# Kernel optimization log

Measured on AMD Instinct MI355X. Metric: run time of the kernel, lower is better.

Reference implementation:

```python
import jax, jax.numpy as jnp
import numpy as np

N = 100000          # nodes
E = 1600000         # edges
D_IN = 128
HID = 256
N_CLASSES = 10
N_GRAPHS = 64


def gcn_conv(x, src, dst, W, b, n_nodes):
    """PyG GCNConv: add self-loops, symmetric deg^{-1/2} normalization, x@W, scatter-add."""
    h = x @ W  # [N, out]
    loop = jnp.arange(n_nodes, dtype=src.dtype)
    src2 = jnp.concatenate([src, loop])
    dst2 = jnp.concatenate([dst, loop])
    deg = jax.ops.segment_sum(jnp.ones(src2.shape[0], x.dtype), dst2, num_segments=n_nodes)
    dinv = jax.lax.rsqrt(deg)  # deg >= 1 thanks to self-loops
    norm = dinv[src2] * dinv[dst2]  # [E+N]
    msg = norm[:, None] * h[src2]   # [E+N, out]
    return jax.ops.segment_sum(msg, dst2, num_segments=n_nodes) + b


def setup_inputs() -> dict:
    key = jax.random.key(0)
    ks = jax.random.split(key, 12)
    x = jax.random.normal(ks[0], (N, D_IN), dtype=jnp.float32)
    edge_index = jax.random.randint(ks[1], (2, E), 0, N, dtype=jnp.int64)
    batch = jnp.sort(jax.random.randint(ks[2], (N,), 0, N_GRAPHS, dtype=jnp.int64))
    def glorot(k, shape):
        lim = float(np.sqrt(6.0 / (shape[0] + shape[1])))
        return jax.random.uniform(k, shape, jnp.float32, -lim, lim)
    W1 = glorot(ks[3], (D_IN, HID));  b1 = jnp.zeros((HID,), jnp.float32)
    W2 = glorot(ks[4], (HID, HID));   b2 = jnp.zeros((HID,), jnp.float32)
    Wf1 = glorot(ks[5], (HID, HID));  bf1 = jnp.zeros((HID,), jnp.float32)
    Wf2 = glorot(ks[6], (HID, N_CLASSES)); bf2 = jnp.zeros((N_CLASSES,), jnp.float32)
    return {"x": x, "edge_index": edge_index, "batch": batch,
            "W1": W1, "b1": b1, "W2": W2, "b2": b2,
            "Wf1": Wf1, "bf1": bf1, "Wf2": Wf2, "bf2": bf2}


def reference(x, edge_index, batch, W1, b1, W2, b2, Wf1, bf1, Wf2, bf2):
    src, dst = edge_index[0], edge_index[1]
    h = jax.nn.relu(gcn_conv(x, src, dst, W1, b1, N))
    h = jax.nn.relu(gcn_conv(h, src, dst, W2, b2, N))
    # global mean pool over graph ids
    summed = jax.ops.segment_sum(h, batch, num_segments=N_GRAPHS)  # [G, HID]
    counts = jax.ops.segment_sum(jnp.ones((N,), h.dtype), batch, num_segments=N_GRAPHS)
    pooled = summed / jnp.maximum(counts, 1.0)[:, None]
    z = jax.nn.relu(pooled @ Wf1 + bf1)
    alpha = jax.nn.softplus(z @ Wf2 + bf2) + 0.001
    return alpha
```

## Files before the change

### kernel.cpp

```cpp
#include <hip/hip_runtime.h>
#include <math.h>

#define NN   100000
#define NE   1600000
#define DIN  128
#define HID  256
#define NG   64
#define NCLS 10

#define NBLK 128
#define EPB  (NE / NBLK)
#define NBUK 512
#define NPB  196

using bf16x8 = __attribute__((ext_vector_type(8))) short;
using f32x4  = __attribute__((ext_vector_type(4))) float;
using f32x2  = __attribute__((ext_vector_type(2))) float;
using u32x2  = __attribute__((ext_vector_type(2))) unsigned int;

static __device__ __forceinline__ unsigned short f2bf(float f) {
    unsigned u = __float_as_uint(f);
    u += 0x7fff + ((u >> 16) & 1);
    return (unsigned short)(u >> 16);
}
static __device__ __forceinline__ float bf2f(unsigned short h) {
    return __uint_as_float(((unsigned)h) << 16);
}

static __device__ __forceinline__ unsigned char f32_to_fp8(float f) {
    float a = fminf(fabsf(f), 448.f);
    unsigned bits = __float_as_uint(a * 0x1p-120f);
    bits += 0x7ffff + ((bits >> 20) & 1);
    unsigned e4 = (bits >> 20) & 0x7f;
    return (unsigned char)(e4 | (f < 0.f ? 0x80u : 0u));
}
#if __has_builtin(__builtin_amdgcn_cvt_pk_f32_fp8)
#define HAVE_CVT_FP8 1
#endif
static __device__ __forceinline__ void fp8x4_to_f32(unsigned u, float* f) {
#ifdef HAVE_CVT_FP8
    f32x2 lo = __builtin_amdgcn_cvt_pk_f32_fp8((int)u, false);
    f32x2 hi = __builtin_amdgcn_cvt_pk_f32_fp8((int)u, true);
    f[0] = lo[0]; f[1] = lo[1]; f[2] = hi[0]; f[3] = hi[1];
#else
#pragma unroll
    for (int k = 0; k < 4; ++k) {
        unsigned b = (u >> (8 * k)) & 0xffu;
        unsigned bits = ((b & 0x80u) << 24) | ((b & 0x7fu) << 20);
        f[k] = __uint_as_float(bits) * 0x1p+120f;
    }
#endif
}


__global__ __launch_bounds__(256) void k_hist(const int* __restrict__ dst,
                                              int* __restrict__ histg) {
    __shared__ int h[NBUK];
    const int t = threadIdx.x;
    for (int i = t; i < NBUK; i += 256) h[i] = 0;
    __syncthreads();
    const int e0 = blockIdx.x * EPB, e1 = e0 + EPB;
    for (int e = e0 + t; e < e1; e += 256)
        atomicAdd(&h[(unsigned)__builtin_nontemporal_load(&dst[e]) / NPB], 1);
    __syncthreads();
    for (int i = t; i < NBUK; i += 256)
        histg[i * NBLK + blockIdx.x] = h[i];
}

__global__ __launch_bounds__(1024) void k_scan64k(int* __restrict__ d) {
    __shared__ int ts[1024];
    const int t = threadIdx.x;
    const int base = t * 64;
    int s = 0;
    for (int i = 0; i < 64; ++i) s += d[base + i];
    ts[t] = s;
    __syncthreads();
    for (int off = 1; off < 1024; off <<= 1) {
        int u = (t >= off) ? ts[t - off] : 0;
        __syncthreads();
        ts[t] += u;
        __syncthreads();
    }
    int run = ts[t] - s;
    for (int i = 0; i < 64; ++i) {
        int v = d[base + i];
        d[base + i] = run;
        run += v;
    }
}

__global__ __launch_bounds__(256) void k_scatter(const int* __restrict__ src,
                                                 const int* __restrict__ dst,
                                                 const int* __restrict__ offg,
                                                 int2* __restrict__ pairs) {
    __shared__ int cur[NBUK];
    const int t = threadIdx.x;
    for (int i = t; i < NBUK; i += 256) cur[i] = offg[i * NBLK + blockIdx.x];
    __syncthreads();
    const int e0 = blockIdx.x * EPB, e1 = e0 + EPB;
    for (int e = e0 + t; e < e1; e += 256) {
        int d = __builtin_nontemporal_load(&dst[e]);
        int sv = __builtin_nontemporal_load(&src[e]);
        int b = (unsigned)d / NPB;
        int p = atomicAdd(&cur[b], 1);
        u32x2 pv; pv.x = (unsigned)sv; pv.y = (unsigned)d;
        __builtin_nontemporal_store(pv, (u32x2*)&pairs[p]);
    }
}

__global__ __launch_bounds__(256) void k_csr(const int2* __restrict__ pairs,
                                             const int* __restrict__ offg,
                                             int* __restrict__ csr,
                                             int* __restrict__ deg,
                                             float* __restrict__ dinv,
                                             int* __restrict__ offs) {
    __shared__ int cnt[NPB];
    __shared__ int loff[256];
    __shared__ int cur[NPB];
    const int b = blockIdx.x, t = threadIdx.x;
    const int s     = offg[b * NBLK];
    const int e_end = (b == NBUK - 1) ? NE : offg[(b + 1) * NBLK];
    const int nb0   = b * NPB;
    const int nnod  = min(NPB, NN - nb0);
    if (t < NPB) cnt[t] = 0;
    __syncthreads();
    for (int e = s + t; e < e_end; e += 256)
        atomicAdd(&cnt[pairs[e].y - nb0], 1);
    __syncthreads();
    int v = (t < NPB) ? cnt[t] : 0;
    loff[t] = v;
    __syncthreads();
    for (int off = 1; off < 256; off <<= 1) {
        int u = (t >= off) ? loff[t - off] : 0;
        __syncthreads();
        loff[t] += u;
        __syncthreads();
    }
    int myoff = loff[t] - v;
    __syncthreads();
    loff[t] = myoff;
    if (t < NPB) cur[t] = 0;
    __syncthreads();
    if (t < nnod) {
        int node = nb0 + t;
        int dg = cnt[t];
        deg[node]  = dg;
        dinv[node] = rsqrtf((float)(dg + 1));
        offs[node] = s + myoff;
    }
    for (int e = s + t; e < e_end; e += 256) {
        int2 pr = pairs[e];
        int li = pr.y - nb0;
        int p = atomicAdd(&cur[li], 1);
        csr[s + loff[li] + p] = pr.x;
    }
}

__global__ void k_counts(const int* __restrict__ batch, float* __restrict__ countsf) {
    int g = threadIdx.x;
    if (g >= NG) return;
    int lo = 0, hi = NN;
    while (lo < hi) { int mid = (lo + hi) >> 1; if (batch[mid] < g) lo = mid + 1; else hi = mid; }
    int lb = lo;
    lo = 0; hi = NN;
    while (lo < hi) { int mid = (lo + hi) >> 1; if (batch[mid] <= g) lo = mid + 1; else hi = mid; }
    countsf[g] = (float)(lo - lb);
}


__global__ void k_cast_x8(const float* __restrict__ x, const float* __restrict__ dinv,
                          unsigned char* __restrict__ xs8, int nq) {
    int i = blockIdx.x * blockDim.x + threadIdx.x;
    if (i >= nq) return;
    int nd = i >> 5;
    int q  = i & 31;
    float dv = dinv[nd];
    const float4 v = *(const float4*)&x[(size_t)nd * DIN + q * 4];
    uchar4 o;
    o.x = f32_to_fp8(v.x * dv); o.y = f32_to_fp8(v.y * dv);
    o.z = f32_to_fp8(v.z * dv); o.w = f32_to_fp8(v.w * dv);
    *(uchar4*)&xs8[(size_t)nd * DIN + q * 4] = o;
}

__global__ void k_cast_wt2(const float* __restrict__ W1, unsigned short* __restrict__ Wt1,
                           const float* __restrict__ W2, unsigned short* __restrict__ Wt2) {
    int i = blockIdx.x * blockDim.x + threadIdx.x;
    if (i < DIN * HID) {
        int k = i >> 8, nc = i & 255;
        Wt1[nc * DIN + k] = f2bf(W1[i]);
    } else if (i < (DIN + HID) * HID) {
        int j = i - DIN * HID;
        int k = j >> 8, nc = j & 255;
        Wt2[nc * HID + k] = f2bf(W2[j]);
    }
}


template <int MODE>
__global__ __launch_bounds__(256) void k_gemm_mfma(const unsigned short* __restrict__ A,
                                                   const unsigned short* __restrict__ Wt,
                                                   const float* __restrict__ dinv,
                                                   const float* __restrict__ bias,
                                                   void* __restrict__ outp,
                                                   const int* __restrict__ batch,
                                                   float* __restrict__ pooled,
                                                   int M, int K) {
    __shared__ unsigned short As[128 * 40];
    __shared__ unsigned short Bs[128 * 40];
    __shared__ float psum[4][128];
    __shared__ int gloc[128];
    const int t = threadIdx.x;
    const int lane = t & 63;
    const int wid = t >> 6;
    const int wr = wid >> 1, wc = wid & 1;
    const int bm = blockIdx.x * 128, bn = blockIdx.y * 128;
    const int lr = lane & 15;
    const int ko = (lane >> 4) << 3;

    f32x4 acc[4][4] = {};

    const int r = t >> 2;
    const int kq = (t & 3) << 3;

    int g0 = 0;
    if (MODE == 2) {
        g0 = batch[bm];
        for (int i = t; i < 4 * 128; i += 256) ((float*)psum)[i] = 0.f;
        if (t < 128) gloc[t] = (bm + t < M) ? (batch[bm + t] - g0) : 0;
    }

    for (int kk = 0; kk < K; kk += 32) {
#pragma unroll
        for (int h = 0; h < 128; h += 64) {
            int row = bm + r + h;
            int4 v = make_int4(0, 0, 0, 0);
            if (row < M) v = *(const int4*)&A[(size_t)row * K + kk + kq];
            *(int4*)&As[(r + h) * 40 + kq] = v;
        }
#pragma unroll
        for (int h = 0; h < 128; h += 64) {
            int nrow = bn + r + h;
            int4 v = *(const int4*)&Wt[(size_t)nrow * K + kk + kq];
            *(int4*)&Bs[(r + h) * 40 + kq] = v;
        }
        __syncthreads();
        bf16x8 af[4], bfr[4];
#pragma unroll
        for (int mf = 0; mf < 4; ++mf)
            af[mf] = *(const bf16x8*)&As[(wr * 64 + mf * 16 + lr) * 40 + ko];
#pragma unroll
        for (int nf = 0; nf < 4; ++nf)
            bfr[nf] = *(const bf16x8*)&Bs[(wc * 64 + nf * 16 + lr) * 40 + ko];
#pragma unroll
        for (int mf = 0; mf < 4; ++mf)
#pragma unroll
            for (int nf = 0; nf < 4; ++nf)
                acc[mf][nf] = __builtin_amdgcn_mfma_f32_16x16x32_bf16(af[mf], bfr[nf], acc[mf][nf], 0, 0, 0);
        __syncthreads();
    }

    if (MODE == 1) {
        unsigned char* out8 = (unsigned char*)outp;
#pragma unroll
        for (int mf = 0; mf < 4; ++mf) {
#pragma unroll
            for (int b = 0; b < 4; ++b) {
                int row = bm + wr * 64 + mf * 16 + (lane >> 4) * 4 + b;
                if (row >= M) continue;
                float dv = dinv[row];
#pragma unroll
                for (int nf = 0; nf < 4; ++nf) {
                    int col = bn + wc * 64 + nf * 16 + lr;
                    float v = fmaxf(acc[mf][nf][b] + bias[col], 0.f);
                    out8[(size_t)row * HID + col] = f32_to_fp8(dv * v);
                }
            }
        }
    } else {
        const int q4 = (lane >> 4) << 2;
#pragma unroll
        for (int nf = 0; nf < 4; ++nf) {
            const int lcol = wc * 64 + nf * 16 + lr;
            const float bb = bias[bn + lcol];
            float run = 0.f; int gcur = 0;
#pragma unroll
            for (int mf = 0; mf < 4; ++mf) {
#pragma unroll
                for (int b = 0; b < 4; ++b) {
                    int lrow = wr * 64 + mf * 16 + q4 + b;
                    if (bm + lrow < M) {
                        int gl = gloc[lrow];
                        float v = fmaxf(acc[mf][nf][b] + bb, 0.f);
                        if (gl != gcur) {
                            if (run != 0.f) {
                                if (gcur < 4) atomicAdd(&psum[gcur][lcol], run);
                                else atomicAdd(&pooled[(size_t)(g0 + gcur) * HID + bn + lcol], run);
                            }
                            run = 0.f; gcur = gl;
                        }
                        run += v;
                    }
                }
            }
            if (run != 0.f) {
                if (gcur < 4) atomicAdd(&psum[gcur][lcol], run);
                else atomicAdd(&pooled[(size_t)(g0 + gcur) * HID + bn + lcol], run);
            }
        }
        __syncthreads();
        for (int i = t; i < 4 * 128; i += 256) {
            int gl = i >> 7, lcol = i & 127;
            int g = g0 + gl;
            float v = psum[gl][lcol];
            if (g < NG && v != 0.f)
                atomicAdd(&pooled[(size_t)g * HID + bn + lcol], v);
        }
    }
}


__global__ __launch_bounds__(256) void k_agg256(const unsigned char* __restrict__ hs,
                                                const int* __restrict__ csr,
                                                const int* __restrict__ offs,
                                                const int* __restrict__ deg,
                                                const float* __restrict__ dinv,
                                                unsigned short* __restrict__ out, int n) {
    int wid = threadIdx.x >> 6, lane = threadIdx.x & 63;
    int node = blockIdx.x * 4 + wid;
    if (node >= n) return;
    int c = lane << 2;
    float a0, a1, a2, a3;
    {
        unsigned u = *(const unsigned*)&hs[(size_t)node * HID + c];
        float f[4]; fp8x4_to_f32(u, f);
        a0 = f[0]; a1 = f[1]; a2 = f[2]; a3 = f[3];
    }
    int s0 = offs[node], cnt = deg[node];
    for (int base = 0; base < cnt; base += 64) {
        int nb = min(64, cnt - base);
        int idx = (lane < nb) ? __builtin_nontemporal_load(&csr[s0 + base + lane]) : 0;
        int i = 0;
        for (; i + 8 <= nb; i += 8) {
            unsigned v[8];
#pragma unroll
            for (int k = 0; k < 8; ++k) {
                int j = __shfl(idx, i + k);
                v[k] = *(const unsigned*)&hs[(size_t)j * HID + c];
            }
#pragma unroll
            for (int k = 0; k < 8; ++k) {
                float f[4]; fp8x4_to_f32(v[k], f);
                a0 += f[0]; a1 += f[1]; a2 += f[2]; a3 += f[3];
            }
        }
        for (; i + 4 <= nb; i += 4) {
            unsigned v[4];
#pragma unroll
            for (int k = 0; k < 4; ++k) {
                int j = __shfl(idx, i + k);
                v[k] = *(const unsigned*)&hs[(size_t)j * HID + c];
            }
#pragma unroll
            for (int k = 0; k < 4; ++k) {
                float f[4]; fp8x4_to_f32(v[k], f);
                a0 += f[0]; a1 += f[1]; a2 += f[2]; a3 += f[3];
            }
        }
        for (; i < nb; ++i) {
            int j = __shfl(idx, i);
            unsigned u = *(const unsigned*)&hs[(size_t)j * HID + c];
            float f[4]; fp8x4_to_f32(u, f);
            a0 += f[0]; a1 += f[1]; a2 += f[2]; a3 += f[3];
        }
    }
    float dv = dinv[node];
    ushort4 r;
    r.x = f2bf(dv * a0); r.y = f2bf(dv * a1);
    r.z = f2bf(dv * a2); r.w = f2bf(dv * a3);
    *(ushort4*)&out[(size_t)node * HID + c] = r;
}


__global__ __launch_bounds__(256) void k_agg128(const unsigned char* __restrict__ xs,
                                                const int* __restrict__ csr,
                                                const int* __restrict__ offs,
                                                const int* __restrict__ deg,
                                                const float* __restrict__ dinv,
                                                unsigned short* __restrict__ out, int n) {
    int wid = threadIdx.x >> 6, lane = threadIdx.x & 63;
    int node = blockIdx.x * 4 + wid;
    if (node >= n) return;
    int half = lane >> 5, l32 = lane & 31;
    int c = l32 << 2;
    float a0 = 0.f, a1 = 0.f, a2 = 0.f, a3 = 0.f;
    if (half == 0) {
        unsigned u = *(const unsigned*)&xs[(size_t)node * DIN + c];
        float f[4]; fp8x4_to_f32(u, f);
        a0 = f[0]; a1 = f[1]; a2 = f[2]; a3 = f[3];
    }
    int s0 = offs[node], cnt = deg[node];
    for (int base = 0; base < cnt; base += 64) {
        int nb = min(64, cnt - base);
        int idx = (lane < nb) ? __builtin_nontemporal_load(&csr[s0 + base + lane]) : 0;
        int i = 0;
        for (; i + 8 <= nb; i += 8) {
            unsigned v[4];
#pragma unroll
            for (int k = 0; k < 4; ++k) {
                int j = __shfl(idx, i + 2 * k + half);
                v[k] = *(const unsigned*)&xs[(size_t)j * DIN + c];
            }
#pragma unroll
            for (int k = 0; k < 4; ++k) {
                float f[4]; fp8x4_to_f32(v[k], f);
                a0 += f[0]; a1 += f[1]; a2 += f[2]; a3 += f[3];
            }
        }
        for (; i < nb; i += 2) {
            int e = i + half;
            int j = __shfl(idx, e < nb ? e : 0);
            if (e < nb) {
                unsigned u = *(const unsigned*)&xs[(size_t)j * DIN + c];
                float f[4]; fp8x4_to_f32(u, f);
                a0 += f[0]; a1 += f[1]; a2 += f[2]; a3 += f[3];
            }
        }
    }
    a0 += __shfl_xor(a0, 32);
    a1 += __shfl_xor(a1, 32);
    a2 += __shfl_xor(a2, 32);
    a3 += __shfl_xor(a3, 32);
    if (half == 0) {
        float dv = dinv[node];
        ushort4 r;
        r.x = f2bf(dv * a0); r.y = f2bf(dv * a1);
        r.z = f2bf(dv * a2); r.w = f2bf(dv * a3);
        *(ushort4*)&out[(size_t)node * DIN + c] = r;
    }
}


__global__ __launch_bounds__(256) void k_mlp(const float* __restrict__ pooled,
                                             const float* __restrict__ countsf,
                                             const float* __restrict__ Wf1,
                                             const float* __restrict__ bf1,
                                             const float* __restrict__ Wf2,
                                             const float* __restrict__ bf2,
                                             float* __restrict__ out) {
    __shared__ float p[HID];
    __shared__ float z[HID];
    int g = blockIdx.x, t = threadIdx.x;
    float cnt = fmaxf(countsf[g], 1.0f);
    p[t] = pooled[g * HID + t] / cnt;
    __syncthreads();
    float accz = bf1[t];
    for (int k = 0; k < HID; ++k)
        accz = fmaf(p[k], Wf1[k * HID + t], accz);
    z[t] = fmaxf(accz, 0.f);
    __syncthreads();
    if (t < NCLS) {
        float o = bf2[t];
        for (int k = 0; k < HID; ++k)
            o = fmaf(z[k], Wf2[k * NCLS + t], o);
        float sp = fmaxf(o, 0.f) + log1pf(expf(-fabsf(o)));
        out[g * NCLS + t] = sp + 0.001f;
    }
}


extern "C" void kernel_launch(void* const* d_in, const int* in_sizes, int n_in,
                              void* d_out, int out_size, void* d_ws, size_t ws_size,
                              hipStream_t stream) {
    const float* x     = (const float*)d_in[0];
    const int*   ei    = (const int*)d_in[1];
    const int*   batch = (const int*)d_in[2];
    const float* W1    = (const float*)d_in[3];
    const float* b1    = (const float*)d_in[4];
    const float* W2    = (const float*)d_in[5];
    const float* b2    = (const float*)d_in[6];
    const float* Wf1   = (const float*)d_in[7];
    const float* bf1   = (const float*)d_in[8];
    const float* Wf2   = (const float*)d_in[9];
    const float* bf2   = (const float*)d_in[10];
    float* out = (float*)d_out;

    const int* srcv = ei;
    const int* dstv = ei + NE;

    char* p = (char*)d_ws;
    auto take = [&](size_t bytes) -> char* {
        char* q = p; p += (bytes + 255) & ~(size_t)255; return q;
    };
    char* big0 = take((size_t)NN * HID * 2);
    char* big1 = take((size_t)NN * HID * 2);
    unsigned char*  xs8 = (unsigned char*)big0;
    unsigned short* xa  = (unsigned short*)(big0 + (size_t)NN * DIN);
    unsigned char*  h8  = (unsigned char*)big1;
    unsigned short* rB  = (unsigned short*)big0;
    int2* pairs = (int2*)big1;
    unsigned short* wt1  = (unsigned short*)take((size_t)DIN * HID * 2);
    unsigned short* wt2  = (unsigned short*)take((size_t)HID * HID * 2);
    int*   histg   = (int*)take((size_t)NBUK * NBLK * 4);
    int*   deg     = (int*)take((size_t)NN * 4);
    int*   offs    = (int*)take((size_t)NN * 4);
    int*   csr     = (int*)take((size_t)NE * 4);
    float* dinv    = (float*)take((size_t)NN * 4);
    float* pooled  = (float*)take((size_t)NG * HID * 4);
    float* countsf = (float*)take((size_t)NG * 4);

    hipMemsetAsync(pooled, 0, (size_t)NG * HID * 4, stream);

    k_hist<<<NBLK, 256, 0, stream>>>(dstv, histg);
    k_scan64k<<<1, 1024, 0, stream>>>(histg);
    k_scatter<<<NBLK, 256, 0, stream>>>(srcv, dstv, histg, pairs);
    k_csr<<<NBUK, 256, 0, stream>>>(pairs, histg, csr, deg, dinv, offs);
    k_counts<<<1, 64, 0, stream>>>(batch, countsf);

    k_cast_x8<<<(NN * 32 + 255) / 256, 256, 0, stream>>>(x, dinv, xs8, NN * 32);
    k_cast_wt2<<<((DIN + HID) * HID + 255) / 256, 256, 0, stream>>>(W1, wt1, W2, wt2);

    dim3 gg((NN + 127) / 128, HID / 128);
    k_agg128<<<(NN + 3) / 4, 256, 0, stream>>>(xs8, csr, offs, deg, dinv, xa, NN);
    k_gemm_mfma<1><<<gg, 256, 0, stream>>>(xa, wt1, dinv, b1, (void*)h8, batch, pooled, NN, DIN);
    k_agg256<<<(NN + 3) / 4, 256, 0, stream>>>(h8, csr, offs, deg, dinv, rB, NN);
    k_gemm_mfma<2><<<gg, 256, 0, stream>>>(rB, wt2, dinv, b2, nullptr, batch, pooled, NN, HID);

    k_mlp<<<NG, 256, 0, stream>>>(pooled, countsf, Wf1, bf1, Wf2, bf2, out);
}
```

Baseline: 368.8 us.

## Parallelize histogram scan across blocks and pack edge pairs into 32-bit

```diff
diff --git a/kernel.cpp b/kernel.cpp
--- a/kernel.cpp
+++ b/kernel.cpp
@@ -12,6 +12,7 @@
 #define EPB  (NE / NBLK)
 #define NBUK 512
 #define NPB  196
+#define NHIST (NBUK * NBLK)
 
 using bf16x8 = __attribute__((ext_vector_type(8))) short;
 using f32x4  = __attribute__((ext_vector_type(4))) float;
@@ -67,32 +68,61 @@
         histg[i * NBLK + blockIdx.x] = h[i];
 }
 
-__global__ __launch_bounds__(1024) void k_scan64k(int* __restrict__ d) {
-    __shared__ int ts[1024];
-    const int t = threadIdx.x;
-    const int base = t * 64;
-    int s = 0;
-    for (int i = 0; i < 64; ++i) s += d[base + i];
-    ts[t] = s;
-    __syncthreads();
-    for (int off = 1; off < 1024; off <<= 1) {
+__global__ __launch_bounds__(256) void k_bsum2(const int* __restrict__ d,
+                                               int* __restrict__ bsum) {
+    __shared__ int sd[256];
+    int t = threadIdx.x;
+    const int4 v = *(const int4*)&d[blockIdx.x * 1024 + t * 4];
+    sd[t] = v.x + v.y + v.z + v.w;
+    __syncthreads();
+    for (int off = 128; off > 0; off >>= 1) {
+        if (t < off) sd[t] += sd[t + off];
+        __syncthreads();
+    }
+    if (t == 0) bsum[blockIdx.x] = sd[0];
+}
+
+__global__ void k_scanb2(const int* __restrict__ bsum, int* __restrict__ boff) {
+    __shared__ int tmp[64];
+    int t = threadIdx.x;
+    int v = bsum[t];
+    tmp[t] = v; __syncthreads();
+    for (int off = 1; off < 64; off <<= 1) {
+        int u = (t >= off) ? tmp[t - off] : 0;
+        __syncthreads();
+        tmp[t] += u;
+        __syncthreads();
+    }
+    boff[t] = tmp[t] - v;
+}
+
+__global__ __launch_bounds__(256) void k_offs2(int* __restrict__ d,
+                                               const int* __restrict__ boff) {
+    __shared__ int ts[256];
+    int t = threadIdx.x;
+    int base = blockIdx.x * 1024 + t * 4;
+    int4 v = *(const int4*)&d[base];
+    int s = v.x + v.y + v.z + v.w;
+    ts[t] = s; __syncthreads();
+    for (int off = 1; off < 256; off <<= 1) {
         int u = (t >= off) ? ts[t - off] : 0;
         __syncthreads();
         ts[t] += u;
         __syncthreads();
     }
-    int run = ts[t] - s;
-    for (int i = 0; i < 64; ++i) {
-        int v = d[base + i];
-        d[base + i] = run;
-        run += v;
-    }
+    int run = ts[t] - s + boff[blockIdx.x];
+    int4 o;
+    o.x = run; run += v.x;
+    o.y = run; run += v.y;
+    o.z = run; run += v.z;
+    o.w = run; run += v.w;
+    *(int4*)&d[base] = o;
 }
 
 __global__ __launch_bounds__(256) void k_scatter(const int* __restrict__ src,
                                                  const int* __restrict__ dst,
                                                  const int* __restrict__ offg,
-                                                 int2* __restrict__ pairs) {
+                                                 unsigned* __restrict__ pairs) {
     __shared__ int cur[NBUK];
     const int t = threadIdx.x;
     for (int i = t; i < NBUK; i += 256) cur[i] = offg[i * NBLK + blockIdx.x];
@@ -102,13 +132,14 @@
         int d = __builtin_nontemporal_load(&dst[e]);
         int sv = __builtin_nontemporal_load(&src[e]);
         int b = (unsigned)d / NPB;
+        int li = d - b * NPB;
+        unsigned pk = ((unsigned)li << 24) | (unsigned)sv;
         int p = atomicAdd(&cur[b], 1);
-        u32x2 pv; pv.x = (unsigned)sv; pv.y = (unsigned)d;
-        __builtin_nontemporal_store(pv, (u32x2*)&pairs[p]);
-    }
-}
-
-__global__ __launch_bounds__(256) void k_csr(const int2* __restrict__ pairs,
+        __builtin_nontemporal_store(pk, &pairs[p]);
+    }
+}
+
+__global__ __launch_bounds__(256) void k_csr(const unsigned* __restrict__ pairs,
                                              const int* __restrict__ offg,
                                              int* __restrict__ csr,
                                              int* __restrict__ deg,
@@ -125,7 +156,7 @@
     if (t < NPB) cnt[t] = 0;
     __syncthreads();
     for (int e = s + t; e < e_end; e += 256)
-        atomicAdd(&cnt[pairs[e].y - nb0], 1);
+        atomicAdd(&cnt[pairs[e] >> 24], 1);
     __syncthreads();
     int v = (t < NPB) ? cnt[t] : 0;
     loff[t] = v;
@@ -149,10 +180,10 @@
         offs[node] = s + myoff;
     }
     for (int e = s + t; e < e_end; e += 256) {
-        int2 pr = pairs[e];
-        int li = pr.y - nb0;
+        unsigned pk = pairs[e];
+        int li = pk >> 24;
         int p = atomicAdd(&cur[li], 1);
-        csr[s + loff[li] + p] = pr.x;
+        csr[s + loff[li] + p] = (int)(pk & 0xffffffu);
     }
 }
 
@@ -497,10 +528,12 @@
     unsigned short* xa  = (unsigned short*)(big0 + (size_t)NN * DIN);
     unsigned char*  h8  = (unsigned char*)big1;
     unsigned short* rB  = (unsigned short*)big0;
-    int2* pairs = (int2*)big1;
+    unsigned* pairs = (unsigned*)big1;
     unsigned short* wt1  = (unsigned short*)take((size_t)DIN * HID * 2);
     unsigned short* wt2  = (unsigned short*)take((size_t)HID * HID * 2);
-    int*   histg   = (int*)take((size_t)NBUK * NBLK * 4);
+    int*   histg   = (int*)take((size_t)NHIST * 4);
+    int*   bsum    = (int*)take(64 * 4);
+    int*   boff    = (int*)take(64 * 4);
     int*   deg     = (int*)take((size_t)NN * 4);
     int*   offs    = (int*)take((size_t)NN * 4);
     int*   csr     = (int*)take((size_t)NE * 4);
@@ -511,7 +544,9 @@
     hipMemsetAsync(pooled, 0, (size_t)NG * HID * 4, stream);
 
     k_hist<<<NBLK, 256, 0, stream>>>(dstv, histg);
-    k_scan64k<<<1, 1024, 0, stream>>>(histg);
+    k_bsum2<<<64, 256, 0, stream>>>(histg, bsum);
+    k_scanb2<<<1, 64, 0, stream>>>(bsum, boff);
+    k_offs2<<<64, 256, 0, stream>>>(histg, boff);
     k_scatter<<<NBLK, 256, 0, stream>>>(srcv, dstv, histg, pairs);
     k_csr<<<NBUK, 256, 0, stream>>>(pairs, histg, csr, deg, dinv, offs);
     k_counts<<<1, 64, 0, stream>>>(batch, countsf);
```

Measured after the change: 341.0 us. -7.5%, faster.
